# Performance work log

Hardware: AMD Instinct MI355X
Metric: run time of the kernel (lower is better)

The kernel has to match this reference:

```python
import jax, jax.numpy as jnp
import numpy as np
from jax import lax


def _sepconv(padded, V, Hk):
    """Per-pixel adaptive separable conv.
    padded: [B,C,H+K-1,W+K-1] (replication-padded frame)
    V, Hk : [B,K,H,W] per-pixel vertical / horizontal 1D kernels
    out[b,c,y,x] = sum_{i,j} padded[b,c,y+i,x+j] * V[b,i,y,x] * Hk[b,j,y,x]
    """
    B, C, Hp, Wp = padded.shape
    K = V.shape[1]
    H, W = Hp - K + 1, Wp - K + 1

    def body(acc, j):
        # columns x+j for all output x: [B,C,Hp,W]
        Pj = lax.dynamic_slice(padded, (0, 0, 0, j), (B, C, Hp, W))
        # vertical windows: [B,C,K,H,W] (K static -> static slices)
        win = jnp.stack([Pj[:, :, i:i + H, :] for i in range(K)], axis=2)
        u = jnp.einsum('bcihw,bihw->bchw', win, V)  # vertical contraction
        acc = acc + u * Hk[:, j][:, None]           # weight by horizontal tap j
        return acc, None

    acc0 = jnp.zeros((B, C, H, W), padded.dtype)
    acc, _ = lax.scan(body, acc0, jnp.arange(K))
    return acc


def setup_inputs() -> dict:
    key = jax.random.key(0)
    ks = jax.random.split(key, 6)
    B, C, H, W, K = 2, 3, 512, 512, 51
    frame0 = jax.random.normal(ks[0], (B, C, H, W), dtype=jnp.float32)
    frame2 = jax.random.normal(ks[1], (B, C, H, W), dtype=jnp.float32)
    V1 = jax.random.uniform(ks[2], (B, K, H, W), dtype=jnp.float32)
    H1 = jax.random.uniform(ks[3], (B, K, H, W), dtype=jnp.float32)
    V2 = jax.random.uniform(ks[4], (B, K, H, W), dtype=jnp.float32)
    H2 = jax.random.uniform(ks[5], (B, K, H, W), dtype=jnp.float32)
    return {"frame0": frame0, "frame2": frame2, "V1": V1, "H1": H1, "V2": V2, "H2": H2}


def reference(frame0, frame2, V1, H1, V2, H2):
    # H=W=512 are multiples of 32, so the %32 zero-padding branch is a no-op.
    K = V1.shape[1]
    p = K // 2  # ReplicationPad2d(kernel_pad)
    rep = lambda x: jnp.pad(x, ((0, 0), (0, 0), (p, p), (p, p)), mode='edge')
    dot1 = _sepconv(rep(frame0), V1, H1)
    dot2 = _sepconv(rep(frame2), V2, H2)
    return dot1 + dot2
```

## Files before the change

kernel.cpp:

```cpp
#include <hip/hip_runtime.h>
#include <stdint.h>

namespace {

typedef _Float16 f16x8 __attribute__((ext_vector_type(8)));
typedef float f32x16 __attribute__((ext_vector_type(16)));

__device__ __forceinline__ uint32_t pkrtz(float a, float b) {
  return __builtin_bit_cast(uint32_t, __builtin_amdgcn_cvt_pkrtz(a, b));
}

constexpr int IMG = 512, K = 51;
constexpr int NT = 256;
constexpr int XB = 64;
constexpr int YB = 16;
constexpr int FSLOTS = 52;
constexpr int FG = 16;
constexpr int HP = 29;
constexpr int NQ = 6;

constexpr int FR_U16 = 3 * FG * FSLOTS * 8;
constexpr int H_U32  = 2 * 2 * 64 * HP;
constexpr int CH_B   = FG * FSLOTS * 16;
constexpr int GR_B   = FSLOTS * 16;

__global__ __launch_bounds__(NT, 2)
__attribute__((amdgpu_waves_per_eu(2, 2)))
void sepconv(const float* __restrict__ fr0, const float* __restrict__ fr2,
             const float* __restrict__ V1, const float* __restrict__ H1,
             const float* __restrict__ V2, const float* __restrict__ H2,
             float* __restrict__ out)
{
  __shared__ __align__(16) uint16_t frL[FR_U16];
  __shared__ uint32_t hL[H_U32];
  uint32_t* fr32 = (uint32_t*)frL;

  const int tid = threadIdx.x;
  const int l   = tid & 63;
  const int w   = tid >> 6;
  const int g   = w & 1;
  const int ypar= w >> 1;
  const int n   = l & 31;
  const int kb  = l >> 5;
  const int x0  = blockIdx.x * XB;
  const int y0  = blockIdx.y * YB;
  const int b   = blockIdx.z;
  const size_t plane = (size_t)IMG * IMG;
  const int xloc = 32 * g + n;

  const int hx = tid & 63, hw = tid >> 6;
  const int hyy = hw >> 1, hhalf = hw & 1;
  const int p0h = 13 * hhalf;
  const int rr0 = tid / 192, c0t = (tid % 192) / 64, pc0 = tid % 64;
  const bool has1 = tid < 128;
  const int t1 = tid + 256;
  const int rr1 = t1 / 192, c1t = (t1 % 192) / 64, pc1 = t1 % 64;

  for (int z = tid; z < 512; z += NT) {
    int row = z & 255, ss = z >> 8;
    hL[row * HP + (ss ? 27 : 0)] = 0u;
  }

  #pragma unroll 1
  for (int f = 0; f < 2; ++f) {
    const float* __restrict__ fr = f ? fr2 : fr0;
    const float* __restrict__ Vf = (f ? V2 : V1) + (size_t)b * K * plane;
    const float* __restrict__ Hf = (f ? H2 : H1) + (size_t)b * K * plane;
    const float* __restrict__ frb = fr + (size_t)b * 3 * plane;

    __syncthreads();

    #pragma unroll 1
    for (int it = 0; it < 39; ++it) {
      int task = tid + NT * it;
      {
        int rr = task / 192, rem = task % 192, c = rem / 64, pc = rem % 64;
        int row = min(max(y0 - 25 + rr, 0), IMG - 1);
        int ca  = min(max(x0 - 25 + 2 * pc, 0), IMG - 1);
        int cb  = min(max(x0 - 25 + 2 * pc + 1, 0), IMG - 1);
        float va = frb[(size_t)c * plane + (size_t)row * IMG + ca];
        float vb = frb[(size_t)c * plane + (size_t)row * IMG + cb];
        int slot = (y0 - 25 + rr + 520) % 52;
        fr32[((c * FG + (pc >> 2)) * FSLOTS + slot) * 4 + (pc & 3)] = pkrtz(va, vb);
      }
    }
    {
      int yH = y0 + hyy;
      int base = (hyy * 64 + hx) * HP;
      #pragma unroll
      for (int m = 0; m < 13; ++m) {
        int p = p0h + m, j0 = 2 * p;
        float a  = Hf[(size_t)j0 * plane + (size_t)yH * IMG + x0 + hx];
        float b2 = (j0 + 1 <= 50)
                 ? Hf[(size_t)(j0 + 1) * plane + (size_t)yH * IMG + x0 + hx] : 0.f;
        hL[base + p + 1] = pkrtz(a, b2);
      }
    }
    __syncthreads();

    uint32_t hcP[13];
    uint32_t fcP[2];

    #pragma unroll 1
    for (int s = 0; s < 8; ++s) {
      const int buf = s & 1;
      const int y = y0 + 2 * s;

      if (s > 0) {
        __syncthreads();
        {
          int slot0 = (y + 25 + rr0 + 520) % 52;
          fr32[((c0t * FG + (pc0 >> 2)) * FSLOTS + slot0) * 4 + (pc0 & 3)] = fcP[0];
          if (has1) {
            int slot1 = (y + 25 + rr1 + 520) % 52;
            fr32[((c1t * FG + (pc1 >> 2)) * FSLOTS + slot1) * 4 + (pc1 & 3)] = fcP[1];
          }
        }
        {
          int base = ((buf * 2 + hyy) * 64 + hx) * HP;
          #pragma unroll
          for (int m = 0; m < 13; ++m)
            hL[base + p0h + m + 1] = hcP[m];
        }
        __syncthreads();
      }

      const int yw = y + ypar;

      const float* vb = Vf + (size_t)yw * IMG + x0 + xloc + (size_t)kb * 4 * plane;
      float v0[8], v1[16], vx[3] = {0.f, 0.f, 0.f};
      #pragma unroll
      for (int r = 0; r < 8; ++r)
        v0[r] = vb[(size_t)((r & 3) + 8 * (r >> 2)) * plane];
      #pragma unroll
      for (int r = 0; r < 16; ++r)
        v1[r] = vb[(size_t)(19 + (r & 3) + 8 * (r >> 2)) * plane];
      if (kb == 0) {
        #pragma unroll
        for (int e = 0; e < 3; ++e) vx[e] = vb[(size_t)(16 + e) * plane];
      }
      float op[3] = {0.f, 0.f, 0.f};
      if (f == 1 && l < 32) {
        #pragma unroll
        for (int c = 0; c < 3; ++c)
          op[c] = out[((size_t)(b * 3 + c) * IMG + yw) * IMG + x0 + xloc];
      }

      uint4 Bq[NQ];
      {
        const uint32_t* hrow = hL + ((buf * 2 + ypar) * 64 + xloc) * HP;
        #pragma unroll
        for (int q = 0; q < NQ; ++q) {
          int j0 = 16 * q + 8 * kb - n;
          int pb = j0 >> 1;
          uint32_t rd[5];
          #pragma unroll
          for (int ww = 0; ww < 5; ++ww) {
            int idx = min(max(pb + ww, -1), 26) + 1;
            rd[ww] = hrow[idx];
          }
          uint32_t fv[4];
          #pragma unroll
          for (int v = 0; v < 4; ++v) {
            uint32_t al = (uint32_t)((((uint64_t)rd[v + 1] << 32) | rd[v]) >> 16);
            fv[v] = (n & 1) ? al : rd[v];
          }
          Bq[q] = make_uint4(fv[0], fv[1], fv[2], fv[3]);
        }
      }

      if (s < 7) {
        int yH = y + 2 + hyy;
        #pragma unroll
        for (int m = 0; m < 13; ++m) {
          int p = p0h + m, j0 = 2 * p;
          float a  = Hf[(size_t)j0 * plane + (size_t)yH * IMG + x0 + hx];
          float b2 = (j0 + 1 <= 50)
                   ? Hf[(size_t)(j0 + 1) * plane + (size_t)yH * IMG + x0 + hx] : 0.f;
          hcP[m] = pkrtz(a, b2);
        }
        {
          int row = min(y + 27 + rr0, IMG - 1);
          int ca  = min(max(x0 - 25 + 2 * pc0, 0), IMG - 1);
          int cb  = min(max(x0 - 25 + 2 * pc0 + 1, 0), IMG - 1);
          fcP[0] = pkrtz(frb[(size_t)c0t * plane + (size_t)row * IMG + ca],
                         frb[(size_t)c0t * plane + (size_t)row * IMG + cb]);
          if (has1) {
            int row1 = min(y + 27 + rr1, IMG - 1);
            int ca1  = min(max(x0 - 25 + 2 * pc1, 0), IMG - 1);
            int cb1  = min(max(x0 - 25 + 2 * pc1 + 1, 0), IMG - 1);
            fcP[1] = pkrtz(frb[(size_t)c1t * plane + (size_t)row1 * IMG + ca1],
                           frb[(size_t)c1t * plane + (size_t)row1 * IMG + cb1]);
          }
        }
      }

      int sA = (yw - 25 + 520) % 52;
      int sB = (yw - 6 + 520) % 52;
      int slotA = sA + n; if (slotA >= 52) slotA -= 52;
      int slotB = sB + n; if (slotB >= 52) slotB -= 52;
      const char* pA0 = (const char*)frL + (4 * g + kb) * GR_B + slotA * 16;
      const char* pA1 = (const char*)frL + (4 * g + kb) * GR_B + slotB * 16;

      float accv[3];
      #pragma unroll
      for (int c = 0; c < 3; ++c) {
        float a = 0.f;
        {
          f32x16 D;
          #pragma unroll
          for (int e = 0; e < 16; ++e) D[e] = 0.f;
          #pragma unroll
          for (int q = 0; q < NQ; ++q) {
            f16x8 A = *(const f16x8*)(pA0 + c * CH_B + q * (2 * GR_B));
            D = __builtin_amdgcn_mfma_f32_32x32x16_f16(
                    A, __builtin_bit_cast(f16x8, Bq[q]), D, 0, 0, 0);
          }
          #pragma unroll
          for (int r = 0; r < 8; ++r) a += v0[r] * D[r];
          if (kb == 0) a += vx[0] * D[8] + vx[1] * D[9] + vx[2] * D[10];
        }
        {
          f32x16 D;
          #pragma unroll
          for (int e = 0; e < 16; ++e) D[e] = 0.f;
          #pragma unroll
          for (int q = 0; q < NQ; ++q) {
            f16x8 A = *(const f16x8*)(pA1 + c * CH_B + q * (2 * GR_B));
            D = __builtin_amdgcn_mfma_f32_32x32x16_f16(
                    A, __builtin_bit_cast(f16x8, Bq[q]), D, 0, 0, 0);
          }
          #pragma unroll
          for (int r = 0; r < 16; ++r) a += v1[r] * D[r];
        }
        accv[c] = a;
      }

      #pragma unroll
      for (int c = 0; c < 3; ++c) {
        float t = accv[c] + __shfl_xor(accv[c], 32, 64);
        if (l < 32) {
          size_t oidx = ((size_t)(b * 3 + c) * IMG + yw) * IMG + x0 + xloc;
          out[oidx] = (f == 0) ? t : (op[c] + t);
        }
      }
    }
  }
}

}

extern "C" void kernel_launch(void* const* d_in, const int* in_sizes, int n_in,
                              void* d_out, int out_size, void* d_ws, size_t ws_size,
                              hipStream_t stream)
{
  const float* frame0 = (const float*)d_in[0];
  const float* frame2 = (const float*)d_in[1];
  const float* V1 = (const float*)d_in[2];
  const float* H1 = (const float*)d_in[3];
  const float* V2 = (const float*)d_in[4];
  const float* H2 = (const float*)d_in[5];
  float* o = (float*)d_out;

  dim3 grid(IMG / XB, IMG / YB, 2);
  dim3 block(NT);
  hipLaunchKernelGGL(sepconv, grid, block, 0, stream,
                     frame0, frame2, V1, H1, V2, H2, o);
}
```

Before: 141.9 us.

## Halve row tile, prefetch V taps one step ahead, single-buffer H in LDS

Shrinks the per-block row tile from 16 to 8, which doubles the grid and raises launch bounds to 3 blocks per CU, and drops the double-buffered H staging in LDS to a single buffer. The V weights for the next step are now loaded into registers a full step ahead and swapped between two register arrays via a manually unrolled step loop. The initial frame fill is batched into three passes of 13 loads so the global reads can overlap. The two MFMA chains per channel are interleaved. The aim is to hide global load latency and raise occupancy, at the cost of more redundant halo loads per output row (51-row window for 8 rows) and higher register pressure.

```diff
diff --git a/kernel.cpp b/kernel.cpp
--- a/kernel.cpp
+++ b/kernel.cpp
@@ -13,19 +13,19 @@
 constexpr int IMG = 512, K = 51;
 constexpr int NT = 256;
 constexpr int XB = 64;
-constexpr int YB = 16;
+constexpr int YB = 8;
+constexpr int NSS = YB / 2;
 constexpr int FSLOTS = 52;
 constexpr int FG = 16;
-constexpr int HP = 29;
+constexpr int HP = 27;
 constexpr int NQ = 6;
 
 constexpr int FR_U16 = 3 * FG * FSLOTS * 8;
-constexpr int H_U32  = 2 * 2 * 64 * HP;
+constexpr int H_U32  = 2 * 64 * HP;
 constexpr int CH_B   = FG * FSLOTS * 16;
 constexpr int GR_B   = FSLOTS * 16;
 
-__global__ __launch_bounds__(NT, 2)
-__attribute__((amdgpu_waves_per_eu(2, 2)))
+__global__ __launch_bounds__(NT, 3)
 void sepconv(const float* __restrict__ fr0, const float* __restrict__ fr2,
              const float* __restrict__ V1, const float* __restrict__ H1,
              const float* __restrict__ V2, const float* __restrict__ H2,
@@ -48,18 +48,16 @@
   const size_t plane = (size_t)IMG * IMG;
   const int xloc = 32 * g + n;
 
-  const int hx = tid & 63, hw = tid >> 6;
-  const int hyy = hw >> 1, hhalf = hw & 1;
+  const int hx = tid & 63, hhalf = (tid >> 6) & 1, hyy = (tid >> 7) & 1;
   const int p0h = 13 * hhalf;
   const int rr0 = tid / 192, c0t = (tid % 192) / 64, pc0 = tid % 64;
   const bool has1 = tid < 128;
   const int t1 = tid + 256;
   const int rr1 = t1 / 192, c1t = (t1 % 192) / 64, pc1 = t1 % 64;
-
-  for (int z = tid; z < 512; z += NT) {
-    int row = z & 255, ss = z >> 8;
-    hL[row * HP + (ss ? 27 : 0)] = 0u;
-  }
+  const int sca0 = min(max(x0 - 25 + 2 * pc0, 0), IMG - 1);
+  const int scb0 = min(max(x0 - 25 + 2 * pc0 + 1, 0), IMG - 1);
+  const int sca1 = min(max(x0 - 25 + 2 * pc1, 0), IMG - 1);
+  const int scb1 = min(max(x0 - 25 + 2 * pc1 + 1, 0), IMG - 1);
 
   #pragma unroll 1
   for (int f = 0; f < 2; ++f) {
@@ -68,87 +66,121 @@
     const float* __restrict__ Hf = (f ? H2 : H1) + (size_t)b * K * plane;
     const float* __restrict__ frb = fr + (size_t)b * 3 * plane;
 
-    __syncthreads();
-
-    #pragma unroll 1
-    for (int it = 0; it < 39; ++it) {
-      int task = tid + NT * it;
-      {
-        int rr = task / 192, rem = task % 192, c = rem / 64, pc = rem % 64;
-        int row = min(max(y0 - 25 + rr, 0), IMG - 1);
-        int ca  = min(max(x0 - 25 + 2 * pc, 0), IMG - 1);
-        int cb  = min(max(x0 - 25 + 2 * pc + 1, 0), IMG - 1);
-        float va = frb[(size_t)c * plane + (size_t)row * IMG + ca];
-        float vb = frb[(size_t)c * plane + (size_t)row * IMG + cb];
-        int slot = (y0 - 25 + rr + 520) % 52;
-        fr32[((c * FG + (pc >> 2)) * FSLOTS + slot) * 4 + (pc & 3)] = pkrtz(va, vb);
-      }
-    }
-    {
-      int yH = y0 + hyy;
-      int base = (hyy * 64 + hx) * HP;
+    float vA[27], vB[27];
+    float ha[13], hb[13], fc[4];
+
+    auto loadV = [&](int s, float (&v)[27]) {
+      const int yw = y0 + 2 * s + ypar;
+      const float* vb = Vf + (size_t)yw * IMG + x0 + xloc + (size_t)kb * 4 * plane;
+      #pragma unroll
+      for (int r = 0; r < 8; ++r)
+        v[r] = vb[(size_t)((r & 3) + 8 * (r >> 2)) * plane];
+      #pragma unroll
+      for (int r = 0; r < 16; ++r)
+        v[8 + r] = vb[(size_t)(19 + (r & 3) + 8 * (r >> 2)) * plane];
+      if (kb == 0) {
+        v[24] = vb[16 * plane]; v[25] = vb[17 * plane]; v[26] = vb[18 * plane];
+      } else { v[24] = v[25] = v[26] = 0.f; }
+    };
+    auto loadCarry = [&](int s) {
+      const int y = y0 + 2 * s;
+      const int yH = y + 2 + hyy;
       #pragma unroll
       for (int m = 0; m < 13; ++m) {
         int p = p0h + m, j0 = 2 * p;
-        float a  = Hf[(size_t)j0 * plane + (size_t)yH * IMG + x0 + hx];
-        float b2 = (j0 + 1 <= 50)
-                 ? Hf[(size_t)(j0 + 1) * plane + (size_t)yH * IMG + x0 + hx] : 0.f;
-        hL[base + p + 1] = pkrtz(a, b2);
+        ha[m] = Hf[(size_t)j0 * plane + (size_t)yH * IMG + x0 + hx];
+        hb[m] = (j0 + 1 <= 50)
+              ? Hf[(size_t)(j0 + 1) * plane + (size_t)yH * IMG + x0 + hx] : 0.f;
+      }
+      int row0 = min(y + 27 + rr0, IMG - 1);
+      const float* rp0 = frb + (size_t)c0t * plane + (size_t)row0 * IMG;
+      fc[0] = rp0[sca0]; fc[1] = rp0[scb0];
+      if (has1) {
+        int row1 = min(y + 27 + rr1, IMG - 1);
+        const float* rp1 = frb + (size_t)c1t * plane + (size_t)row1 * IMG;
+        fc[2] = rp1[sca1]; fc[3] = rp1[scb1];
+      }
+    };
+    auto writeCarry = [&](int s) {
+      const int y = y0 + 2 * s;
+      int slot0 = (y + 25 + rr0 + 520) % 52;
+      fr32[((c0t * FG + (pc0 >> 2)) * FSLOTS + slot0) * 4 + (pc0 & 3)] =
+          pkrtz(fc[0], fc[1]);
+      if (has1) {
+        int slot1 = (y + 25 + rr1 + 520) % 52;
+        fr32[((c1t * FG + (pc1 >> 2)) * FSLOTS + slot1) * 4 + (pc1 & 3)] =
+            pkrtz(fc[2], fc[3]);
+      }
+      #pragma unroll
+      for (int m = 0; m < 13; ++m)
+        hL[(hyy * 64 + hx) * HP + p0h + m] = pkrtz(ha[m], hb[m]);
+    };
+
+    __syncthreads();
+
+    float pha[13], phb[13];
+    {
+      const int yH = y0 + hyy;
+      #pragma unroll
+      for (int m = 0; m < 13; ++m) {
+        int p = p0h + m, j0 = 2 * p;
+        pha[m] = Hf[(size_t)j0 * plane + (size_t)yH * IMG + x0 + hx];
+        phb[m] = (j0 + 1 <= 50)
+               ? Hf[(size_t)(j0 + 1) * plane + (size_t)yH * IMG + x0 + hx] : 0.f;
       }
     }
+    #pragma unroll 1
+    for (int pass = 0; pass < 3; ++pass) {
+      float ta[13], tb[13];
+      #pragma unroll
+      for (int k = 0; k < 13; ++k) {
+        int task = tid + 256 * (pass * 13 + k);
+        int rr = task / 192; int rem = task - rr * 192;
+        int c = rem >> 6, pc = rem & 63;
+        int row = min(max(y0 - 25 + rr, 0), IMG - 1);
+        int ca = min(max(x0 - 25 + 2 * pc, 0), IMG - 1);
+        int cb = min(max(x0 - 25 + 2 * pc + 1, 0), IMG - 1);
+        const float* rp = frb + (size_t)c * plane + (size_t)row * IMG;
+        ta[k] = rp[ca]; tb[k] = rp[cb];
+      }
+      if (pass == 0) {
+        #pragma unroll
+        for (int m = 0; m < 13; ++m)
+          hL[(hyy * 64 + hx) * HP + p0h + m] = pkrtz(pha[m], phb[m]);
+      }
+      #pragma unroll
+      for (int k = 0; k < 13; ++k) {
+        int task = tid + 256 * (pass * 13 + k);
+        int rr = task / 192; int rem = task - rr * 192;
+        int c = rem >> 6, pc = rem & 63;
+        int slot = (y0 - 25 + rr + 520) % 52;
+        fr32[((c * FG + (pc >> 2)) * FSLOTS + slot) * 4 + (pc & 3)] =
+            pkrtz(ta[k], tb[k]);
+      }
+    }
+    loadV(0, vA);
     __syncthreads();
 
-    uint32_t hcP[13];
-    uint32_t fcP[2];
-
-    #pragma unroll 1
-    for (int s = 0; s < 8; ++s) {
-      const int buf = s & 1;
+    auto doSS = [&](int s, float (&vU)[27], float (&vN)[27]) {
       const int y = y0 + 2 * s;
-
       if (s > 0) {
         __syncthreads();
-        {
-          int slot0 = (y + 25 + rr0 + 520) % 52;
-          fr32[((c0t * FG + (pc0 >> 2)) * FSLOTS + slot0) * 4 + (pc0 & 3)] = fcP[0];
-          if (has1) {
-            int slot1 = (y + 25 + rr1 + 520) % 52;
-            fr32[((c1t * FG + (pc1 >> 2)) * FSLOTS + slot1) * 4 + (pc1 & 3)] = fcP[1];
-          }
-        }
-        {
-          int base = ((buf * 2 + hyy) * 64 + hx) * HP;
-          #pragma unroll
-          for (int m = 0; m < 13; ++m)
-            hL[base + p0h + m + 1] = hcP[m];
-        }
+        writeCarry(s);
         __syncthreads();
       }
-
       const int yw = y + ypar;
 
-      const float* vb = Vf + (size_t)yw * IMG + x0 + xloc + (size_t)kb * 4 * plane;
-      float v0[8], v1[16], vx[3] = {0.f, 0.f, 0.f};
-      #pragma unroll
-      for (int r = 0; r < 8; ++r)
-        v0[r] = vb[(size_t)((r & 3) + 8 * (r >> 2)) * plane];
-      #pragma unroll
-      for (int r = 0; r < 16; ++r)
-        v1[r] = vb[(size_t)(19 + (r & 3) + 8 * (r >> 2)) * plane];
-      if (kb == 0) {
-        #pragma unroll
-        for (int e = 0; e < 3; ++e) vx[e] = vb[(size_t)(16 + e) * plane];
-      }
       float op[3] = {0.f, 0.f, 0.f};
       if (f == 1 && l < 32) {
         #pragma unroll
         for (int c = 0; c < 3; ++c)
           op[c] = out[((size_t)(b * 3 + c) * IMG + yw) * IMG + x0 + xloc];
       }
+      if (s + 1 < NSS) { loadV(s + 1, vN); loadCarry(s); }
 
       uint4 Bq[NQ];
       {
-        const uint32_t* hrow = hL + ((buf * 2 + ypar) * 64 + xloc) * HP;
+        const uint32_t* hrow = hL + (ypar * 64 + xloc) * HP;
         #pragma unroll
         for (int q = 0; q < NQ; ++q) {
           int j0 = 16 * q + 8 * kb - n;
@@ -156,42 +188,19 @@
           uint32_t rd[5];
           #pragma unroll
           for (int ww = 0; ww < 5; ++ww) {
-            int idx = min(max(pb + ww, -1), 26) + 1;
-            rd[ww] = hrow[idx];
+            int pw = pb + ww;
+            bool ok = (unsigned)pw <= 25u;
+            uint32_t v = hrow[ok ? pw : 0];
+            rd[ww] = ok ? v : 0u;
           }
           uint32_t fv[4];
           #pragma unroll
-          for (int v = 0; v < 4; ++v) {
-            uint32_t al = (uint32_t)((((uint64_t)rd[v + 1] << 32) | rd[v]) >> 16);
-            fv[v] = (n & 1) ? al : rd[v];
+          for (int v2 = 0; v2 < 4; ++v2) {
+            uint32_t al =
+                (uint32_t)((((uint64_t)rd[v2 + 1] << 32) | rd[v2]) >> 16);
+            fv[v2] = (n & 1) ? al : rd[v2];
           }
           Bq[q] = make_uint4(fv[0], fv[1], fv[2], fv[3]);
-        }
-      }
-
-      if (s < 7) {
-        int yH = y + 2 + hyy;
-        #pragma unroll
-        for (int m = 0; m < 13; ++m) {
-          int p = p0h + m, j0 = 2 * p;
-          float a  = Hf[(size_t)j0 * plane + (size_t)yH * IMG + x0 + hx];
-          float b2 = (j0 + 1 <= 50)
-                   ? Hf[(size_t)(j0 + 1) * plane + (size_t)yH * IMG + x0 + hx] : 0.f;
-          hcP[m] = pkrtz(a, b2);
-        }
-        {
-          int row = min(y + 27 + rr0, IMG - 1);
-          int ca  = min(max(x0 - 25 + 2 * pc0, 0), IMG - 1);
-          int cb  = min(max(x0 - 25 + 2 * pc0 + 1, 0), IMG - 1);
-          fcP[0] = pkrtz(frb[(size_t)c0t * plane + (size_t)row * IMG + ca],
-                         frb[(size_t)c0t * plane + (size_t)row * IMG + cb]);
-          if (has1) {
-            int row1 = min(y + 27 + rr1, IMG - 1);
-            int ca1  = min(max(x0 - 25 + 2 * pc1, 0), IMG - 1);
-            int cb1  = min(max(x0 - 25 + 2 * pc1 + 1, 0), IMG - 1);
-            fcP[1] = pkrtz(frb[(size_t)c1t * plane + (size_t)row1 * IMG + ca1],
-                           frb[(size_t)c1t * plane + (size_t)row1 * IMG + cb1]);
-          }
         }
       }
 
@@ -202,49 +211,38 @@
       const char* pA0 = (const char*)frL + (4 * g + kb) * GR_B + slotA * 16;
       const char* pA1 = (const char*)frL + (4 * g + kb) * GR_B + slotB * 16;
 
-      float accv[3];
       #pragma unroll
       for (int c = 0; c < 3; ++c) {
+        f32x16 D0, D1;
+        #pragma unroll
+        for (int e = 0; e < 16; ++e) { D0[e] = 0.f; D1[e] = 0.f; }
+        #pragma unroll
+        for (int q = 0; q < NQ; ++q) {
+          f16x8 A0 = *(const f16x8*)(pA0 + c * CH_B + q * (2 * GR_B));
+          D0 = __builtin_amdgcn_mfma_f32_32x32x16_f16(
+                   A0, __builtin_bit_cast(f16x8, Bq[q]), D0, 0, 0, 0);
+          f16x8 A1 = *(const f16x8*)(pA1 + c * CH_B + q * (2 * GR_B));
+          D1 = __builtin_amdgcn_mfma_f32_32x32x16_f16(
+                   A1, __builtin_bit_cast(f16x8, Bq[q]), D1, 0, 0, 0);
+        }
         float a = 0.f;
-        {
-          f32x16 D;
-          #pragma unroll
-          for (int e = 0; e < 16; ++e) D[e] = 0.f;
-          #pragma unroll
-          for (int q = 0; q < NQ; ++q) {
-            f16x8 A = *(const f16x8*)(pA0 + c * CH_B + q * (2 * GR_B));
-            D = __builtin_amdgcn_mfma_f32_32x32x16_f16(
-                    A, __builtin_bit_cast(f16x8, Bq[q]), D, 0, 0, 0);
-          }
-          #pragma unroll
-          for (int r = 0; r < 8; ++r) a += v0[r] * D[r];
-          if (kb == 0) a += vx[0] * D[8] + vx[1] * D[9] + vx[2] * D[10];
-        }
-        {
-          f32x16 D;
-          #pragma unroll
-          for (int e = 0; e < 16; ++e) D[e] = 0.f;
-          #pragma unroll
-          for (int q = 0; q < NQ; ++q) {
-            f16x8 A = *(const f16x8*)(pA1 + c * CH_B + q * (2 * GR_B));
-            D = __builtin_amdgcn_mfma_f32_32x32x16_f16(
-                    A, __builtin_bit_cast(f16x8, Bq[q]), D, 0, 0, 0);
-          }
-          #pragma unroll
-          for (int r = 0; r < 16; ++r) a += v1[r] * D[r];
-        }
-        accv[c] = a;
-      }
-
-      #pragma unroll
-      for (int c = 0; c < 3; ++c) {
-        float t = accv[c] + __shfl_xor(accv[c], 32, 64);
+        #pragma unroll
+        for (int r = 0; r < 8; ++r) a += vU[r] * D0[r];
+        if (kb == 0) a += vU[24] * D0[8] + vU[25] * D0[9] + vU[26] * D0[10];
+        #pragma unroll
+        for (int r = 0; r < 16; ++r) a += vU[8 + r] * D1[r];
+        a += __shfl_xor(a, 32, 64);
         if (l < 32) {
           size_t oidx = ((size_t)(b * 3 + c) * IMG + yw) * IMG + x0 + xloc;
-          out[oidx] = (f == 0) ? t : (op[c] + t);
+          out[oidx] = (f == 0) ? a : (op[c] + a);
         }
       }
-    }
+    };
+
+    doSS(0, vA, vB);
+    doSS(1, vB, vA);
+    doSS(2, vA, vB);
+    doSS(3, vB, vA);
   }
 }
 
```

New measurement: 421.7 us. 2.97x slower.
